# Performance work log

Measured on AMD Instinct MI355X. Metric: run time of the kernel, lower is better.

Reference implementation:

```python
import jax, jax.numpy as jnp
import numpy as np
from jax import lax

N, H, W, T = 8, 100, 152, 256
STRIDE = 8
ANCHOR_SIZE = 64.0
PRE_NMS_THRESH = 0.05
PRE_NMS_TOP_N = 1000
NMS_THRESH = 0.6
POST_TOP_N = 100
IMG_H, IMG_W = 800, 1216
BW = (10.0, 10.0, 5.0, 5.0)          # BoxCoder weights (wx, wy, ww, wh)
DWH_CLIP = float(np.log(1000.0 / 16.0))
TO_REMOVE = 1.0


def setup_inputs() -> dict:
    key = jax.random.key(0)
    k1, k2, k3 = jax.random.split(key, 3)
    box_regression = jax.random.normal(k1, (N, 4, H, W), dtype=jnp.float32)
    centerness = jax.random.normal(k2, (N, 1, H, W), dtype=jnp.float32)
    dot_product_logits = jax.random.normal(k3, (N, H * W, T), dtype=jnp.float32)
    # anchor grid matching permute_and_flatten's (H, W, A) row-major ordering
    ys, xs = jnp.meshgrid(jnp.arange(H, dtype=jnp.float32),
                          jnp.arange(W, dtype=jnp.float32), indexing="ij")
    cx = xs.reshape(-1) * STRIDE + STRIDE / 2.0
    cy = ys.reshape(-1) * STRIDE + STRIDE / 2.0
    half = ANCHOR_SIZE / 2.0
    anc = jnp.stack([cx - half, cy - half, cx + half, cy + half], axis=-1)  # [H*W, 4]
    anchors = jnp.broadcast_to(anc, (N, H * W, 4)).astype(jnp.float32)
    return {"box_regression": box_regression, "centerness": centerness,
            "anchors": anchors, "dot_product_logits": dot_product_logits}


def _decode(rel, anc):
    w = anc[..., 2] - anc[..., 0] + TO_REMOVE
    h = anc[..., 3] - anc[..., 1] + TO_REMOVE
    cx = anc[..., 0] + 0.5 * w
    cy = anc[..., 1] + 0.5 * h
    dx = rel[..., 0] / BW[0]
    dy = rel[..., 1] / BW[1]
    dw = jnp.minimum(rel[..., 2] / BW[2], DWH_CLIP)
    dh = jnp.minimum(rel[..., 3] / BW[3], DWH_CLIP)
    pcx = dx * w + cx
    pcy = dy * h + cy
    pw = jnp.exp(dw) * w
    ph = jnp.exp(dh) * h
    return jnp.stack([pcx - 0.5 * pw, pcy - 0.5 * ph,
                      pcx + 0.5 * pw - 1.0, pcy + 0.5 * ph - 1.0], axis=-1)


def _iou_one_vs_all(box, boxes):
    area1 = (box[2] - box[0] + TO_REMOVE) * (box[3] - box[1] + TO_REMOVE)
    area2 = (boxes[:, 2] - boxes[:, 0] + TO_REMOVE) * (boxes[:, 3] - boxes[:, 1] + TO_REMOVE)
    lt = jnp.maximum(box[:2], boxes[:, :2])
    rb = jnp.minimum(box[2:], boxes[:, 2:])
    wh = jnp.maximum(rb - lt + TO_REMOVE, 0.0)
    inter = wh[:, 0] * wh[:, 1]
    return inter / (area1 + area2 - inter)


def _nms_single(boxes, scores):
    # greedy NMS, fixed POST_TOP_N iterations (fpn_post_nms_top_n)
    def step(s, _):
        j = jnp.argmax(s)
        sj = s[j]
        bj = boxes[j]
        flag = (sj > 0).astype(boxes.dtype)
        ious = _iou_one_vs_all(bj, boxes)
        s = jnp.where(ious > NMS_THRESH, 0.0, s).at[j].set(0.0)
        return s, (bj * flag, sj * flag)
    _, (kb, ks) = lax.scan(step, scores, None, length=POST_TOP_N)
    return kb, ks


def reference(box_regression, centerness, anchors, dot_product_logits):
    n, _, h, w = box_regression.shape
    # sigmoid + MEAN token aggregation  -> [N, HWA]
    scores = jax.nn.sigmoid(dot_product_logits).mean(-1)
    # permute_and_flatten: [N,4A,H,W] -> [N, HWA, 4]
    box_reg = box_regression.reshape(n, 1, 4, h, w).transpose(0, 3, 4, 1, 2).reshape(n, -1, 4)
    ctr = jax.nn.sigmoid(centerness.reshape(n, 1, 1, h, w).transpose(0, 3, 4, 1, 2).reshape(n, -1))
    cand = scores > PRE_NMS_THRESH          # threshold on raw aggregated scores
    cls = scores * ctr                      # centerness-weighted score
    masked = jnp.where(cand, cls, 0.0)
    vals, idx = lax.top_k(masked, PRE_NMS_TOP_N)          # per-image top-k candidates
    valid = jnp.take_along_axis(cand, idx, axis=1)        # [N, PRE_NMS_TOP_N]
    sel_reg = jnp.take_along_axis(box_reg, idx[..., None], axis=1)
    sel_anc = jnp.take_along_axis(anchors, idx[..., None], axis=1)
    boxes = _decode(sel_reg, sel_anc)
    # clip_to_image
    boxes = jnp.stack([
        jnp.clip(boxes[..., 0], 0.0, IMG_W - 1.0),
        jnp.clip(boxes[..., 1], 0.0, IMG_H - 1.0),
        jnp.clip(boxes[..., 2], 0.0, IMG_W - 1.0),
        jnp.clip(boxes[..., 3], 0.0, IMG_H - 1.0)], axis=-1)
    vf = valid.astype(boxes.dtype)
    det_scores = jnp.sqrt(jnp.where(valid, vals, 1.0)) * vf   # sqrt of cls*ctr, safe grad
    keep_boxes, keep_scores = jax.vmap(_nms_single)(boxes, det_scores)
    return keep_boxes, keep_scores
```

## Files before the change

kernel.cpp:

```cpp
#include <hip/hip_runtime.h>
#include <math.h>

#define NN 8
#define HH 100
#define WW 152
#define HW (HH*WW)
#define TT 256
#define TOPN 1000
#define POSTN 100
#define NMS_T 0.6f
#define IMGW 1216
#define IMGH 800
#define DWH_CLIP 4.135166556742356f

typedef unsigned long long u64;
typedef unsigned int u32;

__global__ __launch_bounds__(256) void score_kernel(
    const float* __restrict__ logits,
    const float* __restrict__ centerness,
    float* __restrict__ masked)
{
    int wid  = blockIdx.x * 4 + (threadIdx.x >> 6);
    int lane = threadIdx.x & 63;
    const float4 v = *(reinterpret_cast<const float4*>(logits + (size_t)wid * TT) + lane);
    float s = 0.f;
    s += __fdividef(1.f, 1.f + expf(-v.x));
    s += __fdividef(1.f, 1.f + expf(-v.y));
    s += __fdividef(1.f, 1.f + expf(-v.z));
    s += __fdividef(1.f, 1.f + expf(-v.w));
    #pragma unroll
    for (int off = 32; off; off >>= 1) s += __shfl_xor(s, off, 64);
    if (lane == 0) {
        float score = s * (1.0f / 256.0f);
        float c = centerness[wid];
        float ctr = 1.f / (1.f + expf(-c));
        masked[wid] = (score > 0.05f) ? score * ctr : 0.f;
    }
}

__global__ __launch_bounds__(256) void select_nms_kernel(
    const float* __restrict__ masked,
    const float* __restrict__ box_reg,
    float* __restrict__ out)
{
    const int n   = blockIdx.x;
    const int tid = threadIdx.x;
    const int wv  = tid >> 6;
    const int PER = (HW + 255) / 256;

    u32 bits[PER];
    const float* mb = masked + (size_t)n * HW;
    #pragma unroll
    for (int j = 0; j < PER; j++) {
        int e = tid + j * 256;
        bits[j] = (e < HW) ? __float_as_uint(mb[e]) : 0u;
    }

    __shared__ int    parts[2][4];
    __shared__ u64    keys[256];
    __shared__ float4 sbox[256];
    __shared__ float  sscr[256];
    __shared__ float  sarea[256];
    __shared__ u64    smask[256 * 4];
    __shared__ unsigned char ssupp[256];
    __shared__ float4 kbox[POSTN + 4];
    __shared__ int    keep_list[POSTN + 4];
    __shared__ int    s_cnt1, s_cnt2, s_nvalid, s_newkept;

    float* outb = out + (size_t)n * POSTN * 4;
    float* outs = out + (size_t)NN * POSTN * 4 + (size_t)n * POSTN;

    int  kept_total = 0;
    bool done = false;
    u32  thrPrev = 0xFFFFFFFFu;
    int  p = 0;

    for (int b = 0; b < 4 && !done; ++b) {
        const int limit = (b == 3) ? (TOPN - 3 * 256) : 256;

        const int target = 256 * (b + 1) - 1;
        u32 lo = 0u;
        u32 hi = (thrPrev < 0x3F800000u) ? thrPrev : 0x3F800000u;
        while (lo < hi) {
            u32 mid = lo + ((hi - lo) >> 1);
            int c = 0;
            #pragma unroll
            for (int j = 0; j < PER; j++) c += (bits[j] > mid) ? 1 : 0;
            #pragma unroll
            for (int off = 32; off; off >>= 1) c += __shfl_xor(c, off, 64);
            if ((tid & 63) == 0) parts[p][wv] = c;
            __syncthreads();
            int tot = parts[p][0] + parts[p][1] + parts[p][2] + parts[p][3];
            p ^= 1;
            if (tot <= target) hi = mid; else lo = mid + 1;
        }
        const u32 thr = lo;

        if (tid == 0) { s_cnt1 = 0; s_cnt2 = 0; s_nvalid = 0; s_newkept = 0; }
        keys[tid] = 0ull;
        ssupp[tid] = 0;
        __syncthreads();
        #pragma unroll
        for (int j = 0; j < PER; j++) {
            int e = tid + j * 256;
            u32 v = bits[j];
            if (e < HW && v > thr && v < thrPrev) {
                int pos = atomicAdd(&s_cnt1, 1);
                if (pos < 256) keys[pos] = (((u64)v) << 32) | (u32)(~e);
            }
        }
        __syncthreads();
        const int c1 = min(s_cnt1, 256);
        #pragma unroll
        for (int j = 0; j < PER; j++) {
            int e = tid + j * 256;
            if (e < HW && bits[j] == thr) {
                int q = atomicAdd(&s_cnt2, 1);
                if (c1 + q < 256) keys[c1 + q] = (((u64)thr) << 32) | (u32)(~e);
            }
        }
        __syncthreads();

        for (int k = 2; k <= 256; k <<= 1) {
            for (int j2 = k >> 1; j2 > 0; j2 >>= 1) {
                int ixj = tid ^ j2;
                if (ixj > tid) {
                    u64 a = keys[tid], bb = keys[ixj];
                    bool sw = ((tid & k) == 0) ? (a < bb) : (a > bb);
                    if (sw) { keys[tid] = bb; keys[ixj] = a; }
                }
                __syncthreads();
            }
        }

        float4 myb = make_float4(0.f, 0.f, 0.f, 0.f);
        float   myscr = 0.f;
        {
            u64 kk = keys[tid];
            float s = __uint_as_float((u32)(kk >> 32));
            if (s > 0.f) {
                int loc = (int)(~(u32)kk);
                float acx = (float)(loc % WW) * 8.f + 4.f;
                float acy = (float)(loc / WW) * 8.f + 4.f;
                float a0 = acx - 32.f, a1 = acy - 32.f, a2 = acx + 32.f, a3 = acy + 32.f;
                float r0 = box_reg[((size_t)n * 4 + 0) * HW + loc];
                float r1 = box_reg[((size_t)n * 4 + 1) * HW + loc];
                float r2 = box_reg[((size_t)n * 4 + 2) * HW + loc];
                float r3 = box_reg[((size_t)n * 4 + 3) * HW + loc];
                float w  = a2 - a0 + 1.0f;
                float h  = a3 - a1 + 1.0f;
                float cx = a0 + 0.5f * w;
                float cy = a1 + 0.5f * h;
                float dx = r0 / 10.0f;
                float dy = r1 / 10.0f;
                float dw = fminf(r2 / 5.0f, DWH_CLIP);
                float dh = fminf(r3 / 5.0f, DWH_CLIP);
                float pcx = dx * w + cx;
                float pcy = dy * h + cy;
                float pw  = expf(dw) * w;
                float ph  = expf(dh) * h;
                float x1 = pcx - 0.5f * pw;
                float y1 = pcy - 0.5f * ph;
                float x2 = pcx + 0.5f * pw - 1.0f;
                float y2 = pcy + 0.5f * ph - 1.0f;
                myb.x = fminf(fmaxf(x1, 0.f), (float)(IMGW - 1));
                myb.y = fminf(fmaxf(y1, 0.f), (float)(IMGH - 1));
                myb.z = fminf(fmaxf(x2, 0.f), (float)(IMGW - 1));
                myb.w = fminf(fmaxf(y2, 0.f), (float)(IMGH - 1));
                myscr = sqrtf(s);
                if (tid < limit) atomicAdd(&s_nvalid, 1);
            }
            sbox[tid] = myb;
            sscr[tid] = myscr;
            sarea[tid] = (myb.z - myb.x + 1.f) * (myb.w - myb.y + 1.f);
        }
        __syncthreads();

        if (kept_total > 0 && myscr > 0.f) {
            float marea = sarea[tid];
            for (int k = 0; k < kept_total; ++k) {
                float4 kb = kbox[k];
                float ix1 = fmaxf(myb.x, kb.x), iy1 = fmaxf(myb.y, kb.y);
                float ix2 = fminf(myb.z, kb.z), iy2 = fminf(myb.w, kb.w);
                float iw = fmaxf(ix2 - ix1 + 1.f, 0.f), ih = fmaxf(iy2 - iy1 + 1.f, 0.f);
                float inter = iw * ih;
                float karea = (kb.z - kb.x + 1.f) * (kb.w - kb.y + 1.f);
                float iou = inter / (marea + karea - inter);
                if (iou > NMS_T) { ssupp[tid] = 1; break; }
            }
        }

        {
            u64 m0 = 0, m1 = 0, m2 = 0, m3 = 0;
            if (myscr > 0.f) {
                float marea = sarea[tid];
                for (int j = 0; j < 256; ++j) {
                    float4 ob = sbox[j];
                    float ix1 = fmaxf(myb.x, ob.x), iy1 = fmaxf(myb.y, ob.y);
                    float ix2 = fminf(myb.z, ob.z), iy2 = fminf(myb.w, ob.w);
                    float iw = fmaxf(ix2 - ix1 + 1.f, 0.f), ih = fmaxf(iy2 - iy1 + 1.f, 0.f);
                    float inter = iw * ih;
                    float iou = inter / (marea + sarea[j] - inter);
                    if (iou > NMS_T) {
                        u64 bit = 1ull << (j & 63);
                        switch (j >> 6) {
                            case 0: m0 |= bit; break;
                            case 1: m1 |= bit; break;
                            case 2: m2 |= bit; break;
                            default: m3 |= bit; break;
                        }
                    }
                }
            }
            smask[tid * 4 + 0] = m0;
            smask[tid * 4 + 1] = m1;
            smask[tid * 4 + 2] = m2;
            smask[tid * 4 + 3] = m3;
        }
        __syncthreads();

        if (tid < 64) {
            const int l = tid;
            u32 alive = 0;
            #pragma unroll
            for (int k = 0; k < 4; k++) {
                int i = 4 * l + k;
                if (i < limit && sscr[i] > 0.f && ssupp[i] == 0) alive |= (1u << k);
            }
            int newkept = 0;
            while (kept_total + newkept < POSTN) {
                u64 bal = __ballot(alive != 0u);
                if (bal == 0ull) break;
                int w = __ffsll(bal) - 1;
                u32 aw = __shfl(alive, w, 64);
                int c = __ffs(aw) - 1;
                int i = 4 * w + c;
                u64 row = smask[i * 4 + (l >> 4)];
                u32 bits4 = (u32)((row >> ((4 * l) & 63)) & 0xFull);
                alive &= ~bits4;
                if (l == w) alive &= ~(1u << c);
                if (l == 0) keep_list[newkept] = i;
                ++newkept;
            }
            if (tid == 0) s_newkept = newkept;
        }
        __syncthreads();

        const int nk = s_newkept;
        if (tid < nk) {
            int i = keep_list[tid];
            float4 kb = sbox[i];
            int pos = kept_total + tid;
            outb[pos * 4 + 0] = kb.x; outb[pos * 4 + 1] = kb.y;
            outb[pos * 4 + 2] = kb.z; outb[pos * 4 + 3] = kb.w;
            outs[pos] = sscr[i];
            kbox[pos] = kb;
        }
        __syncthreads();

        const int nvalid = s_nvalid;
        kept_total += nk;
        done = (kept_total >= POSTN) || (nvalid < limit);
        thrPrev = thr;
        __syncthreads();
    }

    for (int i = kept_total + tid; i < POSTN; i += 256) {
        outb[i * 4 + 0] = 0.f; outb[i * 4 + 1] = 0.f;
        outb[i * 4 + 2] = 0.f; outb[i * 4 + 3] = 0.f;
        outs[i] = 0.f;
    }
}

extern "C" void kernel_launch(void* const* d_in, const int* in_sizes, int n_in,
                              void* d_out, int out_size, void* d_ws, size_t ws_size,
                              hipStream_t stream) {
    const float* box_reg = (const float*)d_in[0];
    const float* center  = (const float*)d_in[1];
    const float* logits  = (const float*)d_in[3];
    float* out = (float*)d_out;

    float* masked = (float*)d_ws;

    score_kernel<<<(NN * HW) / 4, 256, 0, stream>>>(logits, center, masked);
    select_nms_kernel<<<NN, 256, 0, stream>>>(masked, box_reg, out);
}
```

Measured before the change: 273.5 us.

## Replace binary-search threshold with histogram selection and enlarge NMS batch

The per-image selection kernel now builds a shared-memory histogram over score bit patterns and a suffix-sum prefix, replacing the repeated binary-search threshold passes that needed a block-wide sync per step. Candidates are gathered in batches of up to 512 by histogram bin, bitonic-sorted, and the IoU suppression mask is computed only for the upper triangle, with a wider alive bitmask. The score kernel also processes four rows per wave, so each lane handles four float4 loads and the reduction needs fewer shuffles. In exchange, the selection kernel uses much more shared memory, sorts a larger array, and adds more complicated boundary handling around bin edges.

```diff
diff --git a/kernel.cpp b/kernel.cpp
--- a/kernel.cpp
+++ b/kernel.cpp
@@ -12,30 +12,49 @@
 #define IMGW 1216
 #define IMGH 800
 #define DWH_CLIP 4.135166556742356f
+#define NBINS 8192
+#define BSHIFT 17
+#define CAP 512
 
 typedef unsigned long long u64;
 typedef unsigned int u32;
+
+__device__ __forceinline__ float sigf(float x) {
+    return __fdividef(1.f, 1.f + expf(-x));
+}
 
 __global__ __launch_bounds__(256) void score_kernel(
     const float* __restrict__ logits,
     const float* __restrict__ centerness,
     float* __restrict__ masked)
 {
-    int wid  = blockIdx.x * 4 + (threadIdx.x >> 6);
-    int lane = threadIdx.x & 63;
-    const float4 v = *(reinterpret_cast<const float4*>(logits + (size_t)wid * TT) + lane);
-    float s = 0.f;
-    s += __fdividef(1.f, 1.f + expf(-v.x));
-    s += __fdividef(1.f, 1.f + expf(-v.y));
-    s += __fdividef(1.f, 1.f + expf(-v.z));
-    s += __fdividef(1.f, 1.f + expf(-v.w));
-    #pragma unroll
-    for (int off = 32; off; off >>= 1) s += __shfl_xor(s, off, 64);
-    if (lane == 0) {
+    const int tid  = threadIdx.x;
+    const int lane = tid & 63;
+    const int sub  = lane & 15;
+    const int row  = blockIdx.x * 16 + (tid >> 6) * 4 + (lane >> 4);
+
+    const float4* rp = reinterpret_cast<const float4*>(logits + (size_t)row * TT);
+    float4 a = rp[sub];
+    float4 b = rp[sub + 16];
+    float4 c = rp[sub + 32];
+    float4 d = rp[sub + 48];
+
+    float p0 = ((sigf(a.x) + sigf(a.y)) + sigf(a.z)) + sigf(a.w);
+    float p1 = ((sigf(b.x) + sigf(b.y)) + sigf(b.z)) + sigf(b.w);
+    float p2 = ((sigf(c.x) + sigf(c.y)) + sigf(c.z)) + sigf(c.w);
+    float p3 = ((sigf(d.x) + sigf(d.y)) + sigf(d.z)) + sigf(d.w);
+
+    float s = (p0 + p2) + (p1 + p3);
+    s += __shfl_xor(s, 8, 64);
+    s += __shfl_xor(s, 4, 64);
+    s += __shfl_xor(s, 2, 64);
+    s += __shfl_xor(s, 1, 64);
+
+    if (sub == 0) {
         float score = s * (1.0f / 256.0f);
-        float c = centerness[wid];
-        float ctr = 1.f / (1.f + expf(-c));
-        masked[wid] = (score > 0.05f) ? score * ctr : 0.f;
+        float cv = centerness[row];
+        float ctr = 1.f / (1.f + expf(-cv));
+        masked[row] = (score > 0.05f) ? score * ctr : 0.f;
     }
 }
 
@@ -46,7 +65,6 @@
 {
     const int n   = blockIdx.x;
     const int tid = threadIdx.x;
-    const int wv  = tid >> 6;
     const int PER = (HW + 255) / 256;
 
     u32 bits[PER];
@@ -57,88 +75,128 @@
         bits[j] = (e < HW) ? __float_as_uint(mb[e]) : 0u;
     }
 
-    __shared__ int    parts[2][4];
-    __shared__ u64    keys[256];
-    __shared__ float4 sbox[256];
-    __shared__ float  sscr[256];
-    __shared__ float  sarea[256];
-    __shared__ u64    smask[256 * 4];
-    __shared__ unsigned char ssupp[256];
-    __shared__ float4 kbox[POSTN + 4];
-    __shared__ int    keep_list[POSTN + 4];
-    __shared__ int    s_cnt1, s_cnt2, s_nvalid, s_newkept;
+    __shared__ int    hist[NBINS];
+    __shared__ int    part[256];
+    __shared__ int    lanecum[64];
+    __shared__ u64    keys[CAP];
+    __shared__ float4 sbox[CAP];
+    __shared__ float  sscr[CAP];
+    __shared__ float  sarea[CAP];
+    __shared__ u64    smask[CAP * 8];
+    __shared__ unsigned char ssupp[CAP];
+    __shared__ float4 kbox[POSTN];
+    __shared__ int    keep_list[POSTN];
+    __shared__ int    s_bstar, s_cnt, s_newkept;
+
+    #pragma unroll
+    for (int k = 0; k < NBINS / 256; k++) hist[tid + 256 * k] = 0;
+    __syncthreads();
+    #pragma unroll
+    for (int j = 0; j < PER; j++) {
+        u32 v = bits[j];
+        if (v) atomicAdd(&hist[v >> BSHIFT], 1);
+    }
+    __syncthreads();
+
+    {
+        int s0 = 0;
+        #pragma unroll
+        for (int k = 0; k < 32; k++) s0 += hist[32 * tid + k];
+        part[tid] = s0;
+    }
+    __syncthreads();
+    if (tid < 64) {
+        int g = part[4 * tid] + part[4 * tid + 1] + part[4 * tid + 2] + part[4 * tid + 3];
+        int S = g;
+        #pragma unroll
+        for (int off = 1; off < 64; off <<= 1) {
+            int v = __shfl_down(S, off, 64);
+            if (tid + off < 64) S += v;
+        }
+        lanecum[tid] = S;
+    }
+    __syncthreads();
+    {
+        int cl = tid >> 2, pos = tid & 3;
+        int sfp = lanecum[cl];
+        for (int q = 0; q < pos; q++) sfp -= part[4 * cl + q];
+        int running = sfp - part[tid];
+        for (int k = 31; k >= 0; k--) {
+            int h = hist[32 * tid + k];
+            running += h;
+            hist[32 * tid + k] = running;
+        }
+    }
+    __syncthreads();
+    const int total = hist[0];
 
     float* outb = out + (size_t)n * POSTN * 4;
     float* outs = out + (size_t)NN * POSTN * 4 + (size_t)n * POSTN;
 
-    int  kept_total = 0;
-    bool done = false;
-    u32  thrPrev = 0xFFFFFFFFu;
-    int  p = 0;
+    int  kept_total = 0, consumed = 0;
+    bool done = (total == 0);
+    u32  thrPrevBits = 0x7F800000u;
 
     for (int b = 0; b < 4 && !done; ++b) {
-        const int limit = (b == 3) ? (TOPN - 3 * 256) : 256;
-
-        const int target = 256 * (b + 1) - 1;
-        u32 lo = 0u;
-        u32 hi = (thrPrev < 0x3F800000u) ? thrPrev : 0x3F800000u;
-        while (lo < hi) {
-            u32 mid = lo + ((hi - lo) >> 1);
-            int c = 0;
-            #pragma unroll
-            for (int j = 0; j < PER; j++) c += (bits[j] > mid) ? 1 : 0;
-            #pragma unroll
-            for (int off = 32; off; off >>= 1) c += __shfl_xor(c, off, 64);
-            if ((tid & 63) == 0) parts[p][wv] = c;
-            __syncthreads();
-            int tot = parts[p][0] + parts[p][1] + parts[p][2] + parts[p][3];
-            p ^= 1;
-            if (tot <= target) hi = mid; else lo = mid + 1;
-        }
-        const u32 thr = lo;
-
-        if (tid == 0) { s_cnt1 = 0; s_cnt2 = 0; s_nvalid = 0; s_newkept = 0; }
-        keys[tid] = 0ull;
-        ssupp[tid] = 0;
+        const int X = consumed + CAP;
+        if (tid == 0) s_bstar = 0;
+        __syncthreads();
+        for (int k = 0; k < 32; k++) {
+            int bb = 32 * tid + k;
+            int cb = hist[bb];
+            int pv = (bb == 0) ? 0x7FFFFFFF : hist[bb - 1];
+            if (cb <= X && pv > X) s_bstar = bb;
+        }
+        __syncthreads();
+        int bstar = s_bstar;
+        int Mb = hist[bstar] - consumed;
+        if (Mb <= 0) {
+            if (total - consumed <= 0) break;
+            bstar -= 1;
+            Mb = hist[bstar] - consumed;
+            if (Mb > CAP) Mb = CAP;
+        }
+        const u32 thrLoBits = (u32)bstar << BSHIFT;
+
+        if (tid == 0) s_cnt = 0;
+        keys[tid] = 0ull; keys[tid + 256] = 0ull;
+        ssupp[tid] = 0;   ssupp[tid + 256] = 0;
         __syncthreads();
         #pragma unroll
         for (int j = 0; j < PER; j++) {
-            int e = tid + j * 256;
             u32 v = bits[j];
-            if (e < HW && v > thr && v < thrPrev) {
-                int pos = atomicAdd(&s_cnt1, 1);
-                if (pos < 256) keys[pos] = (((u64)v) << 32) | (u32)(~e);
-            }
-        }
-        __syncthreads();
-        const int c1 = min(s_cnt1, 256);
-        #pragma unroll
-        for (int j = 0; j < PER; j++) {
-            int e = tid + j * 256;
-            if (e < HW && bits[j] == thr) {
-                int q = atomicAdd(&s_cnt2, 1);
-                if (c1 + q < 256) keys[c1 + q] = (((u64)thr) << 32) | (u32)(~e);
-            }
-        }
-        __syncthreads();
-
-        for (int k = 2; k <= 256; k <<= 1) {
+            if (v && v >= thrLoBits && v < thrPrevBits) {
+                int e = tid + j * 256;
+                int pos = atomicAdd(&s_cnt, 1);
+                if (pos < CAP) keys[pos] = (((u64)v) << 32) | (u32)(~e);
+            }
+        }
+        __syncthreads();
+
+        for (int k = 2; k <= CAP; k <<= 1) {
             for (int j2 = k >> 1; j2 > 0; j2 >>= 1) {
-                int ixj = tid ^ j2;
-                if (ixj > tid) {
-                    u64 a = keys[tid], bb = keys[ixj];
-                    bool sw = ((tid & k) == 0) ? (a < bb) : (a > bb);
-                    if (sw) { keys[tid] = bb; keys[ixj] = a; }
+                #pragma unroll
+                for (int hh = 0; hh < 2; hh++) {
+                    int i = tid + hh * 256;
+                    int ixj = i ^ j2;
+                    if (ixj > i) {
+                        u64 a = keys[i], bb2 = keys[ixj];
+                        bool sw = ((i & k) == 0) ? (a < bb2) : (a > bb2);
+                        if (sw) { keys[i] = bb2; keys[ixj] = a; }
+                    }
                 }
                 __syncthreads();
             }
         }
 
-        float4 myb = make_float4(0.f, 0.f, 0.f, 0.f);
-        float   myscr = 0.f;
-        {
-            u64 kk = keys[tid];
+        float4 box1, box2; float area1, area2;
+        #pragma unroll
+        for (int hh = 0; hh < 2; hh++) {
+            int i = tid + hh * 256;
+            u64 kk = keys[i];
             float s = __uint_as_float((u32)(kk >> 32));
+            float4 box = make_float4(0.f, 0.f, 0.f, 0.f);
+            float scr = 0.f;
             if (s > 0.f) {
                 int loc = (int)(~(u32)kk);
                 float acx = (float)(loc % WW) * 8.f + 4.f;
@@ -164,83 +222,94 @@
                 float y1 = pcy - 0.5f * ph;
                 float x2 = pcx + 0.5f * pw - 1.0f;
                 float y2 = pcy + 0.5f * ph - 1.0f;
-                myb.x = fminf(fmaxf(x1, 0.f), (float)(IMGW - 1));
-                myb.y = fminf(fmaxf(y1, 0.f), (float)(IMGH - 1));
-                myb.z = fminf(fmaxf(x2, 0.f), (float)(IMGW - 1));
-                myb.w = fminf(fmaxf(y2, 0.f), (float)(IMGH - 1));
-                myscr = sqrtf(s);
-                if (tid < limit) atomicAdd(&s_nvalid, 1);
-            }
-            sbox[tid] = myb;
-            sscr[tid] = myscr;
-            sarea[tid] = (myb.z - myb.x + 1.f) * (myb.w - myb.y + 1.f);
-        }
-        __syncthreads();
-
-        if (kept_total > 0 && myscr > 0.f) {
-            float marea = sarea[tid];
-            for (int k = 0; k < kept_total; ++k) {
-                float4 kb = kbox[k];
-                float ix1 = fmaxf(myb.x, kb.x), iy1 = fmaxf(myb.y, kb.y);
-                float ix2 = fminf(myb.z, kb.z), iy2 = fminf(myb.w, kb.w);
-                float iw = fmaxf(ix2 - ix1 + 1.f, 0.f), ih = fmaxf(iy2 - iy1 + 1.f, 0.f);
-                float inter = iw * ih;
-                float karea = (kb.z - kb.x + 1.f) * (kb.w - kb.y + 1.f);
-                float iou = inter / (marea + karea - inter);
-                if (iou > NMS_T) { ssupp[tid] = 1; break; }
-            }
-        }
-
-        {
-            u64 m0 = 0, m1 = 0, m2 = 0, m3 = 0;
-            if (myscr > 0.f) {
-                float marea = sarea[tid];
-                for (int j = 0; j < 256; ++j) {
-                    float4 ob = sbox[j];
-                    float ix1 = fmaxf(myb.x, ob.x), iy1 = fmaxf(myb.y, ob.y);
-                    float ix2 = fminf(myb.z, ob.z), iy2 = fminf(myb.w, ob.w);
+                box.x = fminf(fmaxf(x1, 0.f), (float)(IMGW - 1));
+                box.y = fminf(fmaxf(y1, 0.f), (float)(IMGH - 1));
+                box.z = fminf(fmaxf(x2, 0.f), (float)(IMGW - 1));
+                box.w = fminf(fmaxf(y2, 0.f), (float)(IMGH - 1));
+                scr = sqrtf(s);
+            }
+            float ar = (box.z - box.x + 1.f) * (box.w - box.y + 1.f);
+            sbox[i] = box; sscr[i] = scr; sarea[i] = ar;
+            if (hh == 0) { box1 = box; area1 = ar; } else { box2 = box; area2 = ar; }
+        }
+
+        if (kept_total > 0) {
+            #pragma unroll
+            for (int hh = 0; hh < 2; hh++) {
+                int i = tid + hh * 256;
+                float4 myb = (hh == 0) ? box1 : box2;
+                float marea = (hh == 0) ? area1 : area2;
+                if (sscr[i] == 0.f && i >= Mb) continue;
+                for (int k = 0; k < kept_total; ++k) {
+                    float4 kb = kbox[k];
+                    float ix1 = fmaxf(myb.x, kb.x), iy1 = fmaxf(myb.y, kb.y);
+                    float ix2 = fminf(myb.z, kb.z), iy2 = fminf(myb.w, kb.w);
                     float iw = fmaxf(ix2 - ix1 + 1.f, 0.f), ih = fmaxf(iy2 - iy1 + 1.f, 0.f);
                     float inter = iw * ih;
-                    float iou = inter / (marea + sarea[j] - inter);
-                    if (iou > NMS_T) {
-                        u64 bit = 1ull << (j & 63);
-                        switch (j >> 6) {
-                            case 0: m0 |= bit; break;
-                            case 1: m1 |= bit; break;
-                            case 2: m2 |= bit; break;
-                            default: m3 |= bit; break;
-                        }
-                    }
+                    float karea = (kb.z - kb.x + 1.f) * (kb.w - kb.y + 1.f);
+                    float iou = inter / (marea + karea - inter);
+                    if (iou > NMS_T) { ssupp[i] = 1; break; }
                 }
             }
-            smask[tid * 4 + 0] = m0;
-            smask[tid * 4 + 1] = m1;
-            smask[tid * 4 + 2] = m2;
-            smask[tid * 4 + 3] = m3;
-        }
-        __syncthreads();
-
+        }
+        __syncthreads();
+
+        {
+            const int w = tid >> 6;
+            const int r1 = tid, r2 = tid + 256;
+            const bool r1v = (r1 < Mb), r2v = (r2 < Mb);
+            u64 m1[8] = {0,0,0,0,0,0,0,0};
+            u64 m2[8] = {0,0,0,0,0,0,0,0};
+            for (int j = 64 * w + 1; j < Mb; ++j) {
+                float4 ob = sbox[j];
+                float  oa = sarea[j];
+                if (r1v && j > r1) {
+                    float ix1 = fmaxf(box1.x, ob.x), iy1 = fmaxf(box1.y, ob.y);
+                    float ix2 = fminf(box1.z, ob.z), iy2 = fminf(box1.w, ob.w);
+                    float iw = fmaxf(ix2 - ix1 + 1.f, 0.f), ih = fmaxf(iy2 - iy1 + 1.f, 0.f);
+                    float inter = iw * ih;
+                    float iou = inter / (area1 + oa - inter);
+                    if (iou > NMS_T) m1[j >> 6] |= (1ull << (j & 63));
+                }
+                if (r2v && j > r2) {
+                    float ix1 = fmaxf(box2.x, ob.x), iy1 = fmaxf(box2.y, ob.y);
+                    float ix2 = fminf(box2.z, ob.z), iy2 = fminf(box2.w, ob.w);
+                    float iw = fmaxf(ix2 - ix1 + 1.f, 0.f), ih = fmaxf(iy2 - iy1 + 1.f, 0.f);
+                    float inter = iw * ih;
+                    float iou = inter / (area2 + oa - inter);
+                    if (iou > NMS_T) m2[j >> 6] |= (1ull << (j & 63));
+                }
+            }
+            #pragma unroll
+            for (int q = 0; q < 8; q++) {
+                smask[(size_t)r1 * 8 + q] = m1[q];
+                smask[(size_t)r2 * 8 + q] = m2[q];
+            }
+        }
+        __syncthreads();
+
+        int limit = Mb;
+        { int rem = TOPN - consumed; if (limit > rem) limit = rem; }
         if (tid < 64) {
-            const int l = tid;
             u32 alive = 0;
             #pragma unroll
-            for (int k = 0; k < 4; k++) {
-                int i = 4 * l + k;
+            for (int k = 0; k < 8; k++) {
+                int i = 8 * tid + k;
                 if (i < limit && sscr[i] > 0.f && ssupp[i] == 0) alive |= (1u << k);
             }
             int newkept = 0;
             while (kept_total + newkept < POSTN) {
                 u64 bal = __ballot(alive != 0u);
                 if (bal == 0ull) break;
-                int w = __ffsll(bal) - 1;
-                u32 aw = __shfl(alive, w, 64);
-                int c = __ffs(aw) - 1;
-                int i = 4 * w + c;
-                u64 row = smask[i * 4 + (l >> 4)];
-                u32 bits4 = (u32)((row >> ((4 * l) & 63)) & 0xFull);
-                alive &= ~bits4;
-                if (l == w) alive &= ~(1u << c);
-                if (l == 0) keep_list[newkept] = i;
+                int wl = __ffsll((unsigned long long)bal) - 1;
+                u32 aw = __shfl(alive, wl, 64);
+                int c  = __ffs(aw) - 1;
+                int i  = 8 * wl + c;
+                u64 roww = smask[(size_t)i * 8 + (tid >> 3)];
+                u32 byt = (u32)(roww >> ((tid & 7) * 8)) & 0xFFu;
+                alive &= ~byt;
+                if (tid == wl) alive &= ~(1u << c);
+                if (tid == 0) keep_list[newkept] = i;
                 ++newkept;
             }
             if (tid == 0) s_newkept = newkept;
@@ -257,12 +326,10 @@
             outs[pos] = sscr[i];
             kbox[pos] = kb;
         }
-        __syncthreads();
-
-        const int nvalid = s_nvalid;
         kept_total += nk;
-        done = (kept_total >= POSTN) || (nvalid < limit);
-        thrPrev = thr;
+        consumed += Mb;
+        done = (kept_total >= POSTN) || (consumed >= total) || (consumed >= TOPN);
+        thrPrevBits = thrLoBits;
         __syncthreads();
     }
 
@@ -283,6 +350,6 @@
 
     float* masked = (float*)d_ws;
 
-    score_kernel<<<(NN * HW) / 4, 256, 0, stream>>>(logits, center, masked);
+    score_kernel<<<(NN * HW) / 16, 256, 0, stream>>>(logits, center, masked);
     select_nms_kernel<<<NN, 256, 0, stream>>>(masked, box_reg, out);
 }
```

New measurement: 334.0 us. 1.22x slower.
